# Kernel optimization log

Hardware: AMD Instinct MI355X
Metric: run time of the kernel (lower is better)

Reference implementation:

```python
import jax, jax.numpy as jnp
import numpy as np

INPUT_DIM = 1024
CODEBOOK_DIM = 128
CODEBOOK_SIZE = 8192
B, N = 8, 4096


def setup_inputs() -> dict:
    key = jax.random.key(0)
    k1, k2, k3 = jax.random.split(key, 3)
    x = jax.random.normal(k1, (B, N, INPUT_DIM), dtype=jnp.float32)
    # xavier_normal_: std = sqrt(2 / (fan_in + fan_out))
    xavier_std = float(np.sqrt(2.0 / (INPUT_DIM + CODEBOOK_DIM)))
    random_projection = jax.random.normal(k2, (INPUT_DIM, CODEBOOK_DIM), dtype=jnp.float32) * xavier_std
    codebook = jax.random.normal(k3, (CODEBOOK_SIZE, CODEBOOK_DIM), dtype=jnp.float32)
    return {"x": x, "random_projection": random_projection, "codebook": codebook}


def reference(x, random_projection, codebook):
    # random projection: [B, N, D] @ [D, E] -> [B, N, E]
    proj = jnp.einsum("bnd,de->bne", x, random_projection)
    b, n, e = proj.shape
    flat = proj.reshape(b * n, e)  # [BN, E]
    eps = 1e-12  # matches torch F.normalize default eps
    nx = flat / jnp.maximum(jnp.linalg.norm(flat, axis=1, keepdims=True), eps)
    ncb = codebook / jnp.maximum(jnp.linalg.norm(codebook, axis=1, keepdims=True), eps)
    # squared euclidean distances [K, BN]; argmin of d^2 == argmin of cdist
    d2 = (
        jnp.sum(ncb * ncb, axis=1)[:, None]
        + jnp.sum(nx * nx, axis=1)[None, :]
        - 2.0 * (ncb @ nx.T)
    )
    nearest = jnp.argmin(d2, axis=0)  # [BN]
    return nearest.reshape(b, n).astype(jnp.int32)
```

## Files before the change

### kernel.cpp

```cpp
#include <hip/hip_runtime.h>
#include <math.h>
#include <float.h>
#include <limits.h>

#define BN      32768
#define D_IN    1024
#define E_DIM   128
#define CB_N    8192

typedef _Float16 f16x8 __attribute__((ext_vector_type(8)));
typedef _Float16 f16x4 __attribute__((ext_vector_type(4)));
typedef float    f32x4 __attribute__((ext_vector_type(4)));


__global__ __launch_bounds__(256) void pack_cb_kernel(
    const float* __restrict__ cb, _Float16* __restrict__ ph,
    _Float16* __restrict__ pl) {
    __shared__ float L[16][129];
    const int t = threadIdx.x;
    const int g = blockIdx.x;

    const int c = t >> 4, p = t & 15;
    const float4 v0 = *(const float4*)&cb[(size_t)(g * 16 + c) * E_DIM + p * 8];
    const float4 v1 = *(const float4*)&cb[(size_t)(g * 16 + c) * E_DIM + p * 8 + 4];
    float ss = v0.x * v0.x + v0.y * v0.y + v0.z * v0.z + v0.w * v0.w
             + v1.x * v1.x + v1.y * v1.y + v1.z * v1.z + v1.w * v1.w;
#pragma unroll
    for (int m = 1; m < 16; m <<= 1) ss += __shfl_xor(ss, m);
    const float inv = 256.0f / fmaxf(sqrtf(ss), 1e-12f);

    L[c][p * 8 + 0] = v0.x * inv; L[c][p * 8 + 1] = v0.y * inv;
    L[c][p * 8 + 2] = v0.z * inv; L[c][p * 8 + 3] = v0.w * inv;
    L[c][p * 8 + 4] = v1.x * inv; L[c][p * 8 + 5] = v1.y * inv;
    L[c][p * 8 + 6] = v1.z * inv; L[c][p * 8 + 7] = v1.w * inv;
    __syncthreads();

    const int kb = t >> 6, lane = t & 63;
    const int quad = (lane >> 4), col = lane & 15;
    f16x8 h, l;
#pragma unroll
    for (int j = 0; j < 8; ++j) {
        const float v = L[col][kb * 32 + quad * 8 + j];
        const _Float16 hv = (_Float16)v;
        h[j] = hv;
        l[j] = (_Float16)(v - (float)hv);
    }
    const size_t off = ((size_t)(g * 4 + kb) * 64 + lane) * 8;
    *(f16x8*)&ph[off] = h;
    *(f16x8*)&pl[off] = l;
}

__global__ __launch_bounds__(64) void pack_rp_kernel(
    const float* __restrict__ rp, _Float16* __restrict__ rph,
    _Float16* __restrict__ rpl) {
    const int b = blockIdx.x;
    const int kb = b >> 3, nt = b & 7;
    const int lane = threadIdx.x;
    const int quad = lane >> 4, col = lane & 15;
    f16x8 h, l;
#pragma unroll
    for (int j = 0; j < 8; ++j) {
        const float v = rp[(size_t)(kb * 32 + quad * 8 + j) * E_DIM + nt * 16 + col] * 64.0f;
        const _Float16 hv = (_Float16)v;
        h[j] = hv;
        l[j] = (_Float16)(v - (float)hv);
    }
    const size_t off = ((size_t)b * 64 + lane) * 8;
    *(f16x8*)&rph[off] = h;
    *(f16x8*)&rpl[off] = l;
}

#define PAD_ROW 40
#define PPITCH  132

__global__ __launch_bounds__(256, 2) void fused_kernel(
    const float* __restrict__ x,
    const _Float16* __restrict__ rph, const _Float16* __restrict__ rpl,
    const _Float16* __restrict__ ph, const _Float16* __restrict__ pl,
    int* __restrict__ out) {
    __shared__ _Float16 Ah[64 * PAD_ROW];
    __shared__ _Float16 Al[64 * PAD_ROW];
    __shared__ float    P[64 * PPITCH];
    __shared__ float    ls[4][32];
    __shared__ int      li[4][32];

    const int tid  = threadIdx.x;
    const int lane = tid & 63;
    const int w    = tid >> 6;
    const int quad = lane >> 4, col = lane & 15;
    const int qb   = blockIdx.x * 64;

    const int srow = tid >> 3;
    const int skc  = (tid & 7) * 4;

    f32x4 acc[4][2];
#pragma unroll
    for (int mt = 0; mt < 4; ++mt)
#pragma unroll
        for (int h = 0; h < 2; ++h) acc[mt][h] = (f32x4){0.f, 0.f, 0.f, 0.f};

    float4 pre[2];
#pragma unroll
    for (int i = 0; i < 2; ++i)
        pre[i] = *(const float4*)&x[(size_t)(qb + srow + 32 * i) * D_IN + skc];

    for (int kb = 0; kb < 32; ++kb) {
#pragma unroll
        for (int i = 0; i < 2; ++i) {
            const float vv[4] = {pre[i].x, pre[i].y, pre[i].z, pre[i].w};
            f16x4 h4, l4;
#pragma unroll
            for (int j = 0; j < 4; ++j) {
                const float v = vv[j] * 512.0f;
                const _Float16 hv = (_Float16)v;
                h4[j] = hv;
                l4[j] = (_Float16)(v - (float)hv);
            }
            const int base = (srow + 32 * i) * PAD_ROW + skc;
            *(f16x4*)&Ah[base] = h4;
            *(f16x4*)&Al[base] = l4;
        }
        __syncthreads();

        if (kb + 1 < 32) {
#pragma unroll
            for (int i = 0; i < 2; ++i)
                pre[i] = *(const float4*)&x[(size_t)(qb + srow + 32 * i) * D_IN + (kb + 1) * 32 + skc];
        }

        f16x8 bh1[2], bl1[2];
#pragma unroll
        for (int h = 0; h < 2; ++h) {
            const int nt = w * 2 + h;
            const size_t off = ((size_t)(kb * 8 + nt) * 64 + lane) * 8;
            bh1[h] = *(const f16x8*)&rph[off];
            bl1[h] = *(const f16x8*)&rpl[off];
        }

        f16x8 ah1[4], al1[4];
#pragma unroll
        for (int mt = 0; mt < 4; ++mt) {
            const int base = (mt * 16 + col) * PAD_ROW + quad * 8;
            ah1[mt] = *(const f16x8*)&Ah[base];
            al1[mt] = *(const f16x8*)&Al[base];
        }

#pragma unroll
        for (int mt = 0; mt < 4; ++mt)
#pragma unroll
            for (int h = 0; h < 2; ++h)
                acc[mt][h] = __builtin_amdgcn_mfma_f32_16x16x32_f16(ah1[mt], bh1[h], acc[mt][h], 0, 0, 0);
#pragma unroll
        for (int mt = 0; mt < 4; ++mt)
#pragma unroll
            for (int h = 0; h < 2; ++h)
                acc[mt][h] = __builtin_amdgcn_mfma_f32_16x16x32_f16(ah1[mt], bl1[h], acc[mt][h], 0, 0, 0);
#pragma unroll
        for (int mt = 0; mt < 4; ++mt)
#pragma unroll
            for (int h = 0; h < 2; ++h)
                acc[mt][h] = __builtin_amdgcn_mfma_f32_16x16x32_f16(al1[mt], bh1[h], acc[mt][h], 0, 0, 0);

        __syncthreads();
    }

#pragma unroll
    for (int mt = 0; mt < 4; ++mt)
#pragma unroll
        for (int h = 0; h < 2; ++h)
#pragma unroll
            for (int r = 0; r < 4; ++r) {
                const int row = mt * 16 + quad * 4 + r;
                const int cc  = w * 32 + h * 16 + col;
                P[row * PPITCH + cc] = acc[mt][h][r] * (1.0f / 2048.0f);
            }
    __syncthreads();

    const int wq = w >> 1;
    const int wc = w & 1;

    f16x8 ah[2][4], al[2][4];
#pragma unroll
    for (int mt2 = 0; mt2 < 2; ++mt2)
#pragma unroll
        for (int kb = 0; kb < 4; ++kb) {
            const int base = (wq * 32 + mt2 * 16 + col) * PPITCH + kb * 32 + quad * 8;
            const float4 v0 = *(const float4*)&P[base];
            const float4 v1 = *(const float4*)&P[base + 4];
            const float vv[8] = {v0.x, v0.y, v0.z, v0.w, v1.x, v1.y, v1.z, v1.w};
            f16x8 hh, ll;
#pragma unroll
            for (int j = 0; j < 8; ++j) {
                const _Float16 hv = (_Float16)vv[j];
                hh[j] = hv;
                ll[j] = (_Float16)(vv[j] - (float)hv);
            }
            ah[mt2][kb] = hh;
            al[mt2][kb] = ll;
        }

    float bs[8];
    int   bi[8];
#pragma unroll
    for (int s = 0; s < 8; ++s) { bs[s] = -FLT_MAX; bi[s] = 0; }

    const int g0 = wc * 256;

    f16x8 bh[2][4], bl[2][4];
#pragma unroll
    for (int kb = 0; kb < 4; ++kb) {
        const size_t off = ((size_t)(g0 * 4 + kb) * 64 + lane) * 8;
        bh[0][kb] = *(const f16x8*)&ph[off];
        bl[0][kb] = *(const f16x8*)&pl[off];
    }

#pragma unroll 2
    for (int t = 0; t < 256; ++t) {
        const int cur = t & 1, nxt = cur ^ 1;
        if (t + 1 < 256) {
            const int gn = g0 + t + 1;
#pragma unroll
            for (int kb = 0; kb < 4; ++kb) {
                const size_t off = ((size_t)(gn * 4 + kb) * 64 + lane) * 8;
                bh[nxt][kb] = *(const f16x8*)&ph[off];
                bl[nxt][kb] = *(const f16x8*)&pl[off];
            }
        }

        f32x4 sacc[2];
#pragma unroll
        for (int mt2 = 0; mt2 < 2; ++mt2) sacc[mt2] = (f32x4){0.f, 0.f, 0.f, 0.f};

#pragma unroll
        for (int kb = 0; kb < 4; ++kb)
#pragma unroll
            for (int mt2 = 0; mt2 < 2; ++mt2)
                sacc[mt2] = __builtin_amdgcn_mfma_f32_16x16x32_f16(ah[mt2][kb], bh[cur][kb], sacc[mt2], 0, 0, 0);
#pragma unroll
        for (int kb = 0; kb < 4; ++kb)
#pragma unroll
            for (int mt2 = 0; mt2 < 2; ++mt2)
                sacc[mt2] = __builtin_amdgcn_mfma_f32_16x16x32_f16(ah[mt2][kb], bl[cur][kb], sacc[mt2], 0, 0, 0);
#pragma unroll
        for (int kb = 0; kb < 4; ++kb)
#pragma unroll
            for (int mt2 = 0; mt2 < 2; ++mt2)
                sacc[mt2] = __builtin_amdgcn_mfma_f32_16x16x32_f16(al[mt2][kb], bh[cur][kb], sacc[mt2], 0, 0, 0);

        const int code = (g0 + t) * 16 + col;
#pragma unroll
        for (int mt2 = 0; mt2 < 2; ++mt2)
#pragma unroll
            for (int r = 0; r < 4; ++r) {
                const float v = sacc[mt2][r];
                const int s = mt2 * 4 + r;
                if (v > bs[s]) { bs[s] = v; bi[s] = code; }
            }
    }

#pragma unroll
    for (int s = 0; s < 8; ++s) {
#pragma unroll
        for (int m = 1; m < 16; m <<= 1) {
            const float os = __shfl_xor(bs[s], m);
            const int   oi = __shfl_xor(bi[s], m);
            if (os > bs[s] || (os == bs[s] && oi < bi[s])) { bs[s] = os; bi[s] = oi; }
        }
    }

    if (col == 0) {
#pragma unroll
        for (int mt2 = 0; mt2 < 2; ++mt2)
#pragma unroll
            for (int r = 0; r < 4; ++r) {
                ls[w][mt2 * 16 + quad * 4 + r] = bs[mt2 * 4 + r];
                li[w][mt2 * 16 + quad * 4 + r] = bi[mt2 * 4 + r];
            }
    }
    __syncthreads();

    if (tid < 64) {
        const int q   = tid;
        const int wq2 = q >> 5;
        const int q32 = q & 31;
        float s = ls[wq2 * 2 + 0][q32];
        int   i = li[wq2 * 2 + 0][q32];
        const float os = ls[wq2 * 2 + 1][q32];
        if (os > s) { s = os; i = li[wq2 * 2 + 1][q32]; }
        out[qb + q] = i;
    }
}

extern "C" void kernel_launch(void* const* d_in, const int* in_sizes, int n_in,
                              void* d_out, int out_size, void* d_ws, size_t ws_size,
                              hipStream_t stream) {
    const float* x  = (const float*)d_in[0];
    const float* rp = (const float*)d_in[1];
    const float* cb = (const float*)d_in[2];
    int* out = (int*)d_out;

    _Float16* ph  = (_Float16*)d_ws;
    _Float16* pl  = ph  + (size_t)CB_N * E_DIM;
    _Float16* rph = pl  + (size_t)CB_N * E_DIM;
    _Float16* rpl = rph + (size_t)D_IN * E_DIM;

    pack_cb_kernel<<<CB_N / 16, 256, 0, stream>>>(cb, ph, pl);
    pack_rp_kernel<<<256, 64, 0, stream>>>(rp, rph, rpl);
    fused_kernel<<<BN / 64, 256, 0, stream>>>(x, rph, rpl, ph, pl, out);
}
```

Before: 395.6 us.

## Double query tile per block and share codebook tiles via LDS across waves

The fused kernel now handles 128 queries per block instead of 64, with each wave owning 32 queries and scanning the full codebook. Codebook hi/lo tiles are loaded cooperatively into a double-buffered LDS buffer rather than each wave fetching its own half from global memory. This removes the cross-wave argmin merge and the two pack kernels are merged into one launch. In exchange it uses more registers (launch bounds 1), adds a block-wide sync per codebook tile, and halves the grid to 256 blocks.

```diff
diff --git a/kernel.cpp b/kernel.cpp
--- a/kernel.cpp
+++ b/kernel.cpp
@@ -13,101 +13,99 @@
 typedef float    f32x4 __attribute__((ext_vector_type(4)));
 
 
-__global__ __launch_bounds__(256) void pack_cb_kernel(
-    const float* __restrict__ cb, _Float16* __restrict__ ph,
-    _Float16* __restrict__ pl) {
-    __shared__ float L[16][129];
+__global__ __launch_bounds__(256) void pack_kernel(
+    const float* __restrict__ cb, const float* __restrict__ rp,
+    _Float16* __restrict__ ph, _Float16* __restrict__ pl,
+    _Float16* __restrict__ rph, _Float16* __restrict__ rpl) {
     const int t = threadIdx.x;
-    const int g = blockIdx.x;
-
-    const int c = t >> 4, p = t & 15;
-    const float4 v0 = *(const float4*)&cb[(size_t)(g * 16 + c) * E_DIM + p * 8];
-    const float4 v1 = *(const float4*)&cb[(size_t)(g * 16 + c) * E_DIM + p * 8 + 4];
-    float ss = v0.x * v0.x + v0.y * v0.y + v0.z * v0.z + v0.w * v0.w
-             + v1.x * v1.x + v1.y * v1.y + v1.z * v1.z + v1.w * v1.w;
-#pragma unroll
-    for (int m = 1; m < 16; m <<= 1) ss += __shfl_xor(ss, m);
-    const float inv = 256.0f / fmaxf(sqrtf(ss), 1e-12f);
-
-    L[c][p * 8 + 0] = v0.x * inv; L[c][p * 8 + 1] = v0.y * inv;
-    L[c][p * 8 + 2] = v0.z * inv; L[c][p * 8 + 3] = v0.w * inv;
-    L[c][p * 8 + 4] = v1.x * inv; L[c][p * 8 + 5] = v1.y * inv;
-    L[c][p * 8 + 6] = v1.z * inv; L[c][p * 8 + 7] = v1.w * inv;
-    __syncthreads();
-
-    const int kb = t >> 6, lane = t & 63;
-    const int quad = (lane >> 4), col = lane & 15;
-    f16x8 h, l;
-#pragma unroll
-    for (int j = 0; j < 8; ++j) {
-        const float v = L[col][kb * 32 + quad * 8 + j];
-        const _Float16 hv = (_Float16)v;
-        h[j] = hv;
-        l[j] = (_Float16)(v - (float)hv);
-    }
-    const size_t off = ((size_t)(g * 4 + kb) * 64 + lane) * 8;
-    *(f16x8*)&ph[off] = h;
-    *(f16x8*)&pl[off] = l;
+    if (blockIdx.x < 512) {
+        __shared__ float L[16][129];
+        const int g = blockIdx.x;
+        const int c = t >> 4, p = t & 15;
+        const float4 v0 = *(const float4*)&cb[(size_t)(g * 16 + c) * E_DIM + p * 8];
+        const float4 v1 = *(const float4*)&cb[(size_t)(g * 16 + c) * E_DIM + p * 8 + 4];
+        float ss = v0.x * v0.x + v0.y * v0.y + v0.z * v0.z + v0.w * v0.w
+                 + v1.x * v1.x + v1.y * v1.y + v1.z * v1.z + v1.w * v1.w;
+#pragma unroll
+        for (int m = 1; m < 16; m <<= 1) ss += __shfl_xor(ss, m);
+        const float inv = 256.0f / fmaxf(sqrtf(ss), 1e-12f);
+
+        L[c][p * 8 + 0] = v0.x * inv; L[c][p * 8 + 1] = v0.y * inv;
+        L[c][p * 8 + 2] = v0.z * inv; L[c][p * 8 + 3] = v0.w * inv;
+        L[c][p * 8 + 4] = v1.x * inv; L[c][p * 8 + 5] = v1.y * inv;
+        L[c][p * 8 + 6] = v1.z * inv; L[c][p * 8 + 7] = v1.w * inv;
+        __syncthreads();
+
+        const int kb = t >> 6, lane = t & 63;
+        const int quad = (lane >> 4), col = lane & 15;
+        f16x8 h, l;
+#pragma unroll
+        for (int j = 0; j < 8; ++j) {
+            const float v = L[col][kb * 32 + quad * 8 + j];
+            const _Float16 hv = (_Float16)v;
+            h[j] = hv;
+            l[j] = (_Float16)(v - (float)hv);
+        }
+        const size_t off = ((size_t)(g * 4 + kb) * 64 + lane) * 8;
+        *(f16x8*)&ph[off] = h;
+        *(f16x8*)&pl[off] = l;
+    } else {
+        const int w = t >> 6, lane = t & 63;
+        const int b = (blockIdx.x - 512) * 4 + w;
+        const int kb = b >> 3, nt = b & 7;
+        const int quad = lane >> 4, col = lane & 15;
+        f16x8 h, l;
+#pragma unroll
+        for (int j = 0; j < 8; ++j) {
+            const float v = rp[(size_t)(kb * 32 + quad * 8 + j) * E_DIM + nt * 16 + col] * 64.0f;
+            const _Float16 hv = (_Float16)v;
+            h[j] = hv;
+            l[j] = (_Float16)(v - (float)hv);
+        }
+        const size_t off = ((size_t)b * 64 + lane) * 8;
+        *(f16x8*)&rph[off] = h;
+        *(f16x8*)&rpl[off] = l;
+    }
 }
 
-__global__ __launch_bounds__(64) void pack_rp_kernel(
-    const float* __restrict__ rp, _Float16* __restrict__ rph,
-    _Float16* __restrict__ rpl) {
-    const int b = blockIdx.x;
-    const int kb = b >> 3, nt = b & 7;
-    const int lane = threadIdx.x;
-    const int quad = lane >> 4, col = lane & 15;
-    f16x8 h, l;
-#pragma unroll
-    for (int j = 0; j < 8; ++j) {
-        const float v = rp[(size_t)(kb * 32 + quad * 8 + j) * E_DIM + nt * 16 + col] * 64.0f;
-        const _Float16 hv = (_Float16)v;
-        h[j] = hv;
-        l[j] = (_Float16)(v - (float)hv);
-    }
-    const size_t off = ((size_t)b * 64 + lane) * 8;
-    *(f16x8*)&rph[off] = h;
-    *(f16x8*)&rpl[off] = l;
-}
-
 #define PAD_ROW 40
-#define PPITCH  132
-
-__global__ __launch_bounds__(256, 2) void fused_kernel(
+#define HPITCH  132
+
+__global__ __launch_bounds__(256, 1) void fused_kernel(
     const float* __restrict__ x,
     const _Float16* __restrict__ rph, const _Float16* __restrict__ rpl,
     const _Float16* __restrict__ ph, const _Float16* __restrict__ pl,
     int* __restrict__ out) {
-    __shared__ _Float16 Ah[64 * PAD_ROW];
-    __shared__ _Float16 Al[64 * PAD_ROW];
-    __shared__ float    P[64 * PPITCH];
-    __shared__ float    ls[4][32];
-    __shared__ int      li[4][32];
+    __shared__ __align__(16) unsigned char smem[32768];
+    _Float16* Ah = (_Float16*)smem;
+    _Float16* Al = (_Float16*)(smem + 10240);
+    float*    Pq = (float*)smem;
+    _Float16* Bb = (_Float16*)smem;
 
     const int tid  = threadIdx.x;
     const int lane = tid & 63;
     const int w    = tid >> 6;
     const int quad = lane >> 4, col = lane & 15;
-    const int qb   = blockIdx.x * 64;
-
-    const int srow = tid >> 3;
-    const int skc  = (tid & 7) * 4;
-
-    f32x4 acc[4][2];
-#pragma unroll
-    for (int mt = 0; mt < 4; ++mt)
+    const int qb   = blockIdx.x * 128;
+
+    const int srow = tid >> 1;
+    const int scol = (tid & 1) * 16;
+
+    f32x4 acc[8][2];
+#pragma unroll
+    for (int mt = 0; mt < 8; ++mt)
 #pragma unroll
         for (int h = 0; h < 2; ++h) acc[mt][h] = (f32x4){0.f, 0.f, 0.f, 0.f};
 
-    float4 pre[2];
-#pragma unroll
-    for (int i = 0; i < 2; ++i)
-        pre[i] = *(const float4*)&x[(size_t)(qb + srow + 32 * i) * D_IN + skc];
+    float4 pre[4];
+#pragma unroll
+    for (int c = 0; c < 4; ++c)
+        pre[c] = *(const float4*)&x[(size_t)(qb + srow) * D_IN + scol + c * 4];
 
     for (int kb = 0; kb < 32; ++kb) {
 #pragma unroll
-        for (int i = 0; i < 2; ++i) {
-            const float vv[4] = {pre[i].x, pre[i].y, pre[i].z, pre[i].w};
+        for (int c = 0; c < 4; ++c) {
+            const float vv[4] = {pre[c].x, pre[c].y, pre[c].z, pre[c].w};
             f16x4 h4, l4;
 #pragma unroll
             for (int j = 0; j < 4; ++j) {
@@ -116,7 +114,7 @@
                 h4[j] = hv;
                 l4[j] = (_Float16)(v - (float)hv);
             }
-            const int base = (srow + 32 * i) * PAD_ROW + skc;
+            const int base = srow * PAD_ROW + scol + c * 4;
             *(f16x4*)&Ah[base] = h4;
             *(f16x4*)&Al[base] = l4;
         }
@@ -124,8 +122,8 @@
 
         if (kb + 1 < 32) {
 #pragma unroll
-            for (int i = 0; i < 2; ++i)
-                pre[i] = *(const float4*)&x[(size_t)(qb + srow + 32 * i) * D_IN + (kb + 1) * 32 + skc];
+            for (int c = 0; c < 4; ++c)
+                pre[c] = *(const float4*)&x[(size_t)(qb + srow) * D_IN + (kb + 1) * 32 + scol + c * 4];
         }
 
         f16x8 bh1[2], bl1[2];
@@ -137,26 +135,26 @@
             bl1[h] = *(const f16x8*)&rpl[off];
         }
 
-        f16x8 ah1[4], al1[4];
-#pragma unroll
-        for (int mt = 0; mt < 4; ++mt) {
+        f16x8 ah1[8], al1[8];
+#pragma unroll
+        for (int mt = 0; mt < 8; ++mt) {
             const int base = (mt * 16 + col) * PAD_ROW + quad * 8;
             ah1[mt] = *(const f16x8*)&Ah[base];
             al1[mt] = *(const f16x8*)&Al[base];
         }
 
 #pragma unroll
-        for (int mt = 0; mt < 4; ++mt)
+        for (int mt = 0; mt < 8; ++mt)
 #pragma unroll
             for (int h = 0; h < 2; ++h)
                 acc[mt][h] = __builtin_amdgcn_mfma_f32_16x16x32_f16(ah1[mt], bh1[h], acc[mt][h], 0, 0, 0);
 #pragma unroll
-        for (int mt = 0; mt < 4; ++mt)
+        for (int mt = 0; mt < 8; ++mt)
 #pragma unroll
             for (int h = 0; h < 2; ++h)
                 acc[mt][h] = __builtin_amdgcn_mfma_f32_16x16x32_f16(ah1[mt], bl1[h], acc[mt][h], 0, 0, 0);
 #pragma unroll
-        for (int mt = 0; mt < 4; ++mt)
+        for (int mt = 0; mt < 8; ++mt)
 #pragma unroll
             for (int h = 0; h < 2; ++h)
                 acc[mt][h] = __builtin_amdgcn_mfma_f32_16x16x32_f16(al1[mt], bh1[h], acc[mt][h], 0, 0, 0);
@@ -164,98 +162,121 @@
         __syncthreads();
     }
 
-#pragma unroll
-    for (int mt = 0; mt < 4; ++mt)
-#pragma unroll
-        for (int h = 0; h < 2; ++h)
-#pragma unroll
-            for (int r = 0; r < 4; ++r) {
-                const int row = mt * 16 + quad * 4 + r;
-                const int cc  = w * 32 + h * 16 + col;
-                P[row * PPITCH + cc] = acc[mt][h][r] * (1.0f / 2048.0f);
-            }
-    __syncthreads();
-
-    const int wq = w >> 1;
-    const int wc = w & 1;
-
-    f16x8 ah[2][4], al[2][4];
-#pragma unroll
-    for (int mt2 = 0; mt2 < 2; ++mt2)
-#pragma unroll
-        for (int kb = 0; kb < 4; ++kb) {
-            const int base = (wq * 32 + mt2 * 16 + col) * PPITCH + kb * 32 + quad * 8;
-            const float4 v0 = *(const float4*)&P[base];
-            const float4 v1 = *(const float4*)&P[base + 4];
-            const float vv[8] = {v0.x, v0.y, v0.z, v0.w, v1.x, v1.y, v1.z, v1.w};
-            f16x8 hh, ll;
-#pragma unroll
-            for (int j = 0; j < 8; ++j) {
-                const _Float16 hv = (_Float16)vv[j];
-                hh[j] = hv;
-                ll[j] = (_Float16)(vv[j] - (float)hv);
-            }
-            ah[mt2][kb] = hh;
-            al[mt2][kb] = ll;
-        }
+    f16x8 stg[4];
+#pragma unroll
+    for (int r = 0; r < 4; ++r) {
+        const int cc = w * 4 + r;
+        const _Float16* src = (cc < 8) ? &ph[(size_t)0 * 4096 + cc * 512 + lane * 8]
+                                       : &pl[(size_t)0 * 4096 + (cc - 8) * 512 + lane * 8];
+        stg[r] = *(const f16x8*)src;
+    }
+
+    f16x8 ahF[2][4], alF[2][4];
+#pragma unroll
+    for (int i = 0; i < 4; ++i) {
+#pragma unroll
+        for (int m2 = 0; m2 < 2; ++m2) {
+            const int mt = i * 2 + m2;
+#pragma unroll
+            for (int h = 0; h < 2; ++h)
+#pragma unroll
+                for (int r = 0; r < 4; ++r)
+                    Pq[(m2 * 16 + quad * 4 + r) * HPITCH + w * 32 + h * 16 + col]
+                        = acc[mt][h][r] * (1.0f / 2048.0f);
+        }
+        __syncthreads();
+        if (w == i) {
+#pragma unroll
+            for (int mt2 = 0; mt2 < 2; ++mt2)
+#pragma unroll
+                for (int kbb = 0; kbb < 4; ++kbb) {
+                    const int base = (mt2 * 16 + col) * HPITCH + kbb * 32 + quad * 8;
+                    const float4 v0 = *(const float4*)&Pq[base];
+                    const float4 v1 = *(const float4*)&Pq[base + 4];
+                    const float vv[8] = {v0.x, v0.y, v0.z, v0.w, v1.x, v1.y, v1.z, v1.w};
+                    f16x8 hh, ll;
+#pragma unroll
+                    for (int j = 0; j < 8; ++j) {
+                        const _Float16 hv = (_Float16)vv[j];
+                        hh[j] = hv;
+                        ll[j] = (_Float16)(vv[j] - (float)hv);
+                    }
+                    ahF[mt2][kbb] = hh;
+                    alF[mt2][kbb] = ll;
+                }
+        }
+        __syncthreads();
+    }
 
     float bs[8];
     int   bi[8];
 #pragma unroll
     for (int s = 0; s < 8; ++s) { bs[s] = -FLT_MAX; bi[s] = 0; }
 
-    const int g0 = wc * 256;
-
-    f16x8 bh[2][4], bl[2][4];
-#pragma unroll
-    for (int kb = 0; kb < 4; ++kb) {
-        const size_t off = ((size_t)(g0 * 4 + kb) * 64 + lane) * 8;
-        bh[0][kb] = *(const f16x8*)&ph[off];
-        bl[0][kb] = *(const f16x8*)&pl[off];
-    }
-
-#pragma unroll 2
+#pragma unroll
+    for (int r = 0; r < 4; ++r) {
+        const int cc = w * 4 + r;
+        *(f16x8*)&Bb[cc * 512 + lane * 8] = stg[r];
+    }
+    __syncthreads();
+
     for (int t = 0; t < 256; ++t) {
-        const int cur = t & 1, nxt = cur ^ 1;
+        f16x8 nxt[4];
         if (t + 1 < 256) {
-            const int gn = g0 + t + 1;
-#pragma unroll
-            for (int kb = 0; kb < 4; ++kb) {
-                const size_t off = ((size_t)(gn * 4 + kb) * 64 + lane) * 8;
-                bh[nxt][kb] = *(const f16x8*)&ph[off];
-                bl[nxt][kb] = *(const f16x8*)&pl[off];
-            }
-        }
-
-        f32x4 sacc[2];
-#pragma unroll
-        for (int mt2 = 0; mt2 < 2; ++mt2) sacc[mt2] = (f32x4){0.f, 0.f, 0.f, 0.f};
-
-#pragma unroll
-        for (int kb = 0; kb < 4; ++kb)
-#pragma unroll
-            for (int mt2 = 0; mt2 < 2; ++mt2)
-                sacc[mt2] = __builtin_amdgcn_mfma_f32_16x16x32_f16(ah[mt2][kb], bh[cur][kb], sacc[mt2], 0, 0, 0);
-#pragma unroll
-        for (int kb = 0; kb < 4; ++kb)
-#pragma unroll
-            for (int mt2 = 0; mt2 < 2; ++mt2)
-                sacc[mt2] = __builtin_amdgcn_mfma_f32_16x16x32_f16(ah[mt2][kb], bl[cur][kb], sacc[mt2], 0, 0, 0);
-#pragma unroll
-        for (int kb = 0; kb < 4; ++kb)
-#pragma unroll
-            for (int mt2 = 0; mt2 < 2; ++mt2)
-                sacc[mt2] = __builtin_amdgcn_mfma_f32_16x16x32_f16(al[mt2][kb], bh[cur][kb], sacc[mt2], 0, 0, 0);
-
-        const int code = (g0 + t) * 16 + col;
-#pragma unroll
-        for (int mt2 = 0; mt2 < 2; ++mt2)
 #pragma unroll
             for (int r = 0; r < 4; ++r) {
-                const float v = sacc[mt2][r];
-                const int s = mt2 * 4 + r;
-                if (v > bs[s]) { bs[s] = v; bi[s] = code; }
-            }
+                const int cc = w * 4 + r;
+                const _Float16* src = (cc < 8)
+                    ? &ph[(size_t)(t + 1) * 4096 + cc * 512 + lane * 8]
+                    : &pl[(size_t)(t + 1) * 4096 + (cc - 8) * 512 + lane * 8];
+                nxt[r] = *(const f16x8*)src;
+            }
+        }
+
+        const int bufo = (t & 1) * 8192;
+#pragma unroll
+        for (int ct = 0; ct < 2; ++ct) {
+            f16x8 bh[4], bl[4];
+#pragma unroll
+            for (int kbb = 0; kbb < 4; ++kbb) {
+                bh[kbb] = *(const f16x8*)&Bb[bufo + (ct * 4 + kbb) * 512 + lane * 8];
+                bl[kbb] = *(const f16x8*)&Bb[bufo + 4096 + (ct * 4 + kbb) * 512 + lane * 8];
+            }
+
+            f32x4 s0 = (f32x4){0.f, 0.f, 0.f, 0.f};
+            f32x4 s1 = (f32x4){0.f, 0.f, 0.f, 0.f};
+#pragma unroll
+            for (int kbb = 0; kbb < 4; ++kbb) {
+                s0 = __builtin_amdgcn_mfma_f32_16x16x32_f16(ahF[0][kbb], bh[kbb], s0, 0, 0, 0);
+                s1 = __builtin_amdgcn_mfma_f32_16x16x32_f16(ahF[1][kbb], bh[kbb], s1, 0, 0, 0);
+            }
+#pragma unroll
+            for (int kbb = 0; kbb < 4; ++kbb) {
+                s0 = __builtin_amdgcn_mfma_f32_16x16x32_f16(ahF[0][kbb], bl[kbb], s0, 0, 0, 0);
+                s1 = __builtin_amdgcn_mfma_f32_16x16x32_f16(ahF[1][kbb], bl[kbb], s1, 0, 0, 0);
+            }
+#pragma unroll
+            for (int kbb = 0; kbb < 4; ++kbb) {
+                s0 = __builtin_amdgcn_mfma_f32_16x16x32_f16(alF[0][kbb], bh[kbb], s0, 0, 0, 0);
+                s1 = __builtin_amdgcn_mfma_f32_16x16x32_f16(alF[1][kbb], bh[kbb], s1, 0, 0, 0);
+            }
+
+            const int code = (t * 2 + ct) * 16 + col;
+#pragma unroll
+            for (int r = 0; r < 4; ++r) {
+                if (s0[r] > bs[r])     { bs[r] = s0[r];     bi[r] = code; }
+                if (s1[r] > bs[4 + r]) { bs[4 + r] = s1[r]; bi[4 + r] = code; }
+            }
+        }
+
+        if (t + 1 < 256) {
+#pragma unroll
+            for (int r = 0; r < 4; ++r) {
+                const int cc = w * 4 + r;
+                *(f16x8*)&Bb[((t + 1) & 1) * 8192 + cc * 512 + lane * 8] = nxt[r];
+            }
+        }
+        __syncthreads();
     }
 
 #pragma unroll
@@ -272,22 +293,8 @@
 #pragma unroll
         for (int mt2 = 0; mt2 < 2; ++mt2)
 #pragma unroll
-            for (int r = 0; r < 4; ++r) {
-                ls[w][mt2 * 16 + quad * 4 + r] = bs[mt2 * 4 + r];
-                li[w][mt2 * 16 + quad * 4 + r] = bi[mt2 * 4 + r];
-            }
-    }
-    __syncthreads();
-
-    if (tid < 64) {
-        const int q   = tid;
-        const int wq2 = q >> 5;
-        const int q32 = q & 31;
-        float s = ls[wq2 * 2 + 0][q32];
-        int   i = li[wq2 * 2 + 0][q32];
-        const float os = ls[wq2 * 2 + 1][q32];
-        if (os > s) { s = os; i = li[wq2 * 2 + 1][q32]; }
-        out[qb + q] = i;
+            for (int r = 0; r < 4; ++r)
+                out[qb + w * 32 + mt2 * 16 + quad * 4 + r] = bi[mt2 * 4 + r];
     }
 }
 
@@ -304,7 +311,6 @@
     _Float16* rph = pl  + (size_t)CB_N * E_DIM;
     _Float16* rpl = rph + (size_t)D_IN * E_DIM;
 
-    pack_cb_kernel<<<CB_N / 16, 256, 0, stream>>>(cb, ph, pl);
-    pack_rp_kernel<<<256, 64, 0, stream>>>(rp, rph, rpl);
-    fused_kernel<<<BN / 64, 256, 0, stream>>>(x, rph, rpl, ph, pl, out);
+    pack_kernel<<<576, 256, 0, stream>>>(cb, rp, ph, pl, rph, rpl);
+    fused_kernel<<<BN / 128, 256, 0, stream>>>(x, rph, rpl, ph, pl, out);
 }
```

Result: slower. 438.8 us (+10.9%).

## Split codebook across all four waves and merge pack kernels into one

Applied to the files above, without the earlier changes.

Each wave now scores all 64 query rows against a quarter of the codebook, instead of 32 rows against half. Each codebook fragment loaded from global memory then feeds 4 M-tiles rather than 2, so total codebook traffic per block is halved. The cost is more registers (16 A fragments per wave plus 16 best-score slots) and a 4-way final merge. The two pack kernels are also fused into one launch, and the first codebook prefetch is moved before the barrier.

```diff
diff --git a/kernel.cpp b/kernel.cpp
--- a/kernel.cpp
+++ b/kernel.cpp
@@ -13,61 +13,59 @@
 typedef float    f32x4 __attribute__((ext_vector_type(4)));
 
 
-__global__ __launch_bounds__(256) void pack_cb_kernel(
-    const float* __restrict__ cb, _Float16* __restrict__ ph,
-    _Float16* __restrict__ pl) {
-    __shared__ float L[16][129];
+__global__ __launch_bounds__(256) void pack_kernel(
+    const float* __restrict__ cb, const float* __restrict__ rp,
+    _Float16* __restrict__ ph, _Float16* __restrict__ pl,
+    _Float16* __restrict__ rph, _Float16* __restrict__ rpl) {
     const int t = threadIdx.x;
-    const int g = blockIdx.x;
-
-    const int c = t >> 4, p = t & 15;
-    const float4 v0 = *(const float4*)&cb[(size_t)(g * 16 + c) * E_DIM + p * 8];
-    const float4 v1 = *(const float4*)&cb[(size_t)(g * 16 + c) * E_DIM + p * 8 + 4];
-    float ss = v0.x * v0.x + v0.y * v0.y + v0.z * v0.z + v0.w * v0.w
-             + v1.x * v1.x + v1.y * v1.y + v1.z * v1.z + v1.w * v1.w;
-#pragma unroll
-    for (int m = 1; m < 16; m <<= 1) ss += __shfl_xor(ss, m);
-    const float inv = 256.0f / fmaxf(sqrtf(ss), 1e-12f);
-
-    L[c][p * 8 + 0] = v0.x * inv; L[c][p * 8 + 1] = v0.y * inv;
-    L[c][p * 8 + 2] = v0.z * inv; L[c][p * 8 + 3] = v0.w * inv;
-    L[c][p * 8 + 4] = v1.x * inv; L[c][p * 8 + 5] = v1.y * inv;
-    L[c][p * 8 + 6] = v1.z * inv; L[c][p * 8 + 7] = v1.w * inv;
-    __syncthreads();
-
-    const int kb = t >> 6, lane = t & 63;
-    const int quad = (lane >> 4), col = lane & 15;
-    f16x8 h, l;
-#pragma unroll
-    for (int j = 0; j < 8; ++j) {
-        const float v = L[col][kb * 32 + quad * 8 + j];
-        const _Float16 hv = (_Float16)v;
-        h[j] = hv;
-        l[j] = (_Float16)(v - (float)hv);
-    }
-    const size_t off = ((size_t)(g * 4 + kb) * 64 + lane) * 8;
-    *(f16x8*)&ph[off] = h;
-    *(f16x8*)&pl[off] = l;
-}
-
-__global__ __launch_bounds__(64) void pack_rp_kernel(
-    const float* __restrict__ rp, _Float16* __restrict__ rph,
-    _Float16* __restrict__ rpl) {
-    const int b = blockIdx.x;
-    const int kb = b >> 3, nt = b & 7;
-    const int lane = threadIdx.x;
-    const int quad = lane >> 4, col = lane & 15;
-    f16x8 h, l;
-#pragma unroll
-    for (int j = 0; j < 8; ++j) {
-        const float v = rp[(size_t)(kb * 32 + quad * 8 + j) * E_DIM + nt * 16 + col] * 64.0f;
-        const _Float16 hv = (_Float16)v;
-        h[j] = hv;
-        l[j] = (_Float16)(v - (float)hv);
-    }
-    const size_t off = ((size_t)b * 64 + lane) * 8;
-    *(f16x8*)&rph[off] = h;
-    *(f16x8*)&rpl[off] = l;
+    if (blockIdx.x < 512) {
+        __shared__ float L[16][129];
+        const int g = blockIdx.x;
+        const int c = t >> 4, p = t & 15;
+        const float4 v0 = *(const float4*)&cb[(size_t)(g * 16 + c) * E_DIM + p * 8];
+        const float4 v1 = *(const float4*)&cb[(size_t)(g * 16 + c) * E_DIM + p * 8 + 4];
+        float ss = v0.x * v0.x + v0.y * v0.y + v0.z * v0.z + v0.w * v0.w
+                 + v1.x * v1.x + v1.y * v1.y + v1.z * v1.z + v1.w * v1.w;
+#pragma unroll
+        for (int m = 1; m < 16; m <<= 1) ss += __shfl_xor(ss, m);
+        const float inv = 256.0f / fmaxf(sqrtf(ss), 1e-12f);
+
+        L[c][p * 8 + 0] = v0.x * inv; L[c][p * 8 + 1] = v0.y * inv;
+        L[c][p * 8 + 2] = v0.z * inv; L[c][p * 8 + 3] = v0.w * inv;
+        L[c][p * 8 + 4] = v1.x * inv; L[c][p * 8 + 5] = v1.y * inv;
+        L[c][p * 8 + 6] = v1.z * inv; L[c][p * 8 + 7] = v1.w * inv;
+        __syncthreads();
+
+        const int kb = t >> 6, lane = t & 63;
+        const int quad = (lane >> 4), col = lane & 15;
+        f16x8 h, l;
+#pragma unroll
+        for (int j = 0; j < 8; ++j) {
+            const float v = L[col][kb * 32 + quad * 8 + j];
+            const _Float16 hv = (_Float16)v;
+            h[j] = hv;
+            l[j] = (_Float16)(v - (float)hv);
+        }
+        const size_t off = ((size_t)(g * 4 + kb) * 64 + lane) * 8;
+        *(f16x8*)&ph[off] = h;
+        *(f16x8*)&pl[off] = l;
+    } else {
+        const int w = t >> 6, lane = t & 63;
+        const int b = (blockIdx.x - 512) * 4 + w;
+        const int kb = b >> 3, nt = b & 7;
+        const int quad = lane >> 4, col = lane & 15;
+        f16x8 h, l;
+#pragma unroll
+        for (int j = 0; j < 8; ++j) {
+            const float v = rp[(size_t)(kb * 32 + quad * 8 + j) * E_DIM + nt * 16 + col] * 64.0f;
+            const _Float16 hv = (_Float16)v;
+            h[j] = hv;
+            l[j] = (_Float16)(v - (float)hv);
+        }
+        const size_t off = ((size_t)b * 64 + lane) * 8;
+        *(f16x8*)&rph[off] = h;
+        *(f16x8*)&rpl[off] = l;
+    }
 }
 
 #define PAD_ROW 40
@@ -81,8 +79,8 @@
     __shared__ _Float16 Ah[64 * PAD_ROW];
     __shared__ _Float16 Al[64 * PAD_ROW];
     __shared__ float    P[64 * PPITCH];
-    __shared__ float    ls[4][32];
-    __shared__ int      li[4][32];
+    __shared__ float    ls[4][64];
+    __shared__ int      li[4][64];
 
     const int tid  = threadIdx.x;
     const int lane = tid & 63;
@@ -169,22 +167,26 @@
 #pragma unroll
         for (int h = 0; h < 2; ++h)
 #pragma unroll
-            for (int r = 0; r < 4; ++r) {
-                const int row = mt * 16 + quad * 4 + r;
-                const int cc  = w * 32 + h * 16 + col;
-                P[row * PPITCH + cc] = acc[mt][h][r] * (1.0f / 2048.0f);
-            }
+            for (int r = 0; r < 4; ++r)
+                P[(mt * 16 + quad * 4 + r) * PPITCH + w * 32 + h * 16 + col]
+                    = acc[mt][h][r] * (1.0f / 2048.0f);
+
+    const int g0 = w * 128;
+    f16x8 bh[2][4], bl[2][4];
+#pragma unroll
+    for (int kb = 0; kb < 4; ++kb) {
+        const size_t off = ((size_t)(g0 * 4 + kb) * 64 + lane) * 8;
+        bh[0][kb] = *(const f16x8*)&ph[off];
+        bl[0][kb] = *(const f16x8*)&pl[off];
+    }
     __syncthreads();
 
-    const int wq = w >> 1;
-    const int wc = w & 1;
-
-    f16x8 ah[2][4], al[2][4];
-#pragma unroll
-    for (int mt2 = 0; mt2 < 2; ++mt2)
-#pragma unroll
-        for (int kb = 0; kb < 4; ++kb) {
-            const int base = (wq * 32 + mt2 * 16 + col) * PPITCH + kb * 32 + quad * 8;
+    f16x8 ahF[4][4], alF[4][4];
+#pragma unroll
+    for (int mt = 0; mt < 4; ++mt)
+#pragma unroll
+        for (int kbb = 0; kbb < 4; ++kbb) {
+            const int base = (mt * 16 + col) * PPITCH + kbb * 32 + quad * 8;
             const float4 v0 = *(const float4*)&P[base];
             const float4 v1 = *(const float4*)&P[base + 4];
             const float vv[8] = {v0.x, v0.y, v0.z, v0.w, v1.x, v1.y, v1.z, v1.w};
@@ -195,29 +197,19 @@
                 hh[j] = hv;
                 ll[j] = (_Float16)(vv[j] - (float)hv);
             }
-            ah[mt2][kb] = hh;
-            al[mt2][kb] = ll;
-        }
-
-    float bs[8];
-    int   bi[8];
-#pragma unroll
-    for (int s = 0; s < 8; ++s) { bs[s] = -FLT_MAX; bi[s] = 0; }
-
-    const int g0 = wc * 256;
-
-    f16x8 bh[2][4], bl[2][4];
-#pragma unroll
-    for (int kb = 0; kb < 4; ++kb) {
-        const size_t off = ((size_t)(g0 * 4 + kb) * 64 + lane) * 8;
-        bh[0][kb] = *(const f16x8*)&ph[off];
-        bl[0][kb] = *(const f16x8*)&pl[off];
-    }
+            ahF[mt][kbb] = hh;
+            alF[mt][kbb] = ll;
+        }
+
+    float bs[16];
+    int   bi[16];
+#pragma unroll
+    for (int s = 0; s < 16; ++s) { bs[s] = -FLT_MAX; bi[s] = 0; }
 
 #pragma unroll 2
-    for (int t = 0; t < 256; ++t) {
+    for (int t = 0; t < 128; ++t) {
         const int cur = t & 1, nxt = cur ^ 1;
-        if (t + 1 < 256) {
+        if (t + 1 < 128) {
             const int gn = g0 + t + 1;
 #pragma unroll
             for (int kb = 0; kb < 4; ++kb) {
@@ -227,39 +219,39 @@
             }
         }
 
-        f32x4 sacc[2];
-#pragma unroll
-        for (int mt2 = 0; mt2 < 2; ++mt2) sacc[mt2] = (f32x4){0.f, 0.f, 0.f, 0.f};
+        f32x4 sacc[4];
+#pragma unroll
+        for (int mt = 0; mt < 4; ++mt) sacc[mt] = (f32x4){0.f, 0.f, 0.f, 0.f};
 
 #pragma unroll
         for (int kb = 0; kb < 4; ++kb)
 #pragma unroll
-            for (int mt2 = 0; mt2 < 2; ++mt2)
-                sacc[mt2] = __builtin_amdgcn_mfma_f32_16x16x32_f16(ah[mt2][kb], bh[cur][kb], sacc[mt2], 0, 0, 0);
+            for (int mt = 0; mt < 4; ++mt)
+                sacc[mt] = __builtin_amdgcn_mfma_f32_16x16x32_f16(ahF[mt][kb], bh[cur][kb], sacc[mt], 0, 0, 0);
 #pragma unroll
         for (int kb = 0; kb < 4; ++kb)
 #pragma unroll
-            for (int mt2 = 0; mt2 < 2; ++mt2)
-                sacc[mt2] = __builtin_amdgcn_mfma_f32_16x16x32_f16(ah[mt2][kb], bl[cur][kb], sacc[mt2], 0, 0, 0);
+            for (int mt = 0; mt < 4; ++mt)
+                sacc[mt] = __builtin_amdgcn_mfma_f32_16x16x32_f16(ahF[mt][kb], bl[cur][kb], sacc[mt], 0, 0, 0);
 #pragma unroll
         for (int kb = 0; kb < 4; ++kb)
 #pragma unroll
-            for (int mt2 = 0; mt2 < 2; ++mt2)
-                sacc[mt2] = __builtin_amdgcn_mfma_f32_16x16x32_f16(al[mt2][kb], bh[cur][kb], sacc[mt2], 0, 0, 0);
+            for (int mt = 0; mt < 4; ++mt)
+                sacc[mt] = __builtin_amdgcn_mfma_f32_16x16x32_f16(alF[mt][kb], bh[cur][kb], sacc[mt], 0, 0, 0);
 
         const int code = (g0 + t) * 16 + col;
 #pragma unroll
-        for (int mt2 = 0; mt2 < 2; ++mt2)
+        for (int mt = 0; mt < 4; ++mt)
 #pragma unroll
             for (int r = 0; r < 4; ++r) {
-                const float v = sacc[mt2][r];
-                const int s = mt2 * 4 + r;
+                const float v = sacc[mt][r];
+                const int s = mt * 4 + r;
                 if (v > bs[s]) { bs[s] = v; bi[s] = code; }
             }
     }
 
 #pragma unroll
-    for (int s = 0; s < 8; ++s) {
+    for (int s = 0; s < 16; ++s) {
 #pragma unroll
         for (int m = 1; m < 16; m <<= 1) {
             const float os = __shfl_xor(bs[s], m);
@@ -270,24 +262,24 @@
 
     if (col == 0) {
 #pragma unroll
-        for (int mt2 = 0; mt2 < 2; ++mt2)
+        for (int mt = 0; mt < 4; ++mt)
 #pragma unroll
             for (int r = 0; r < 4; ++r) {
-                ls[w][mt2 * 16 + quad * 4 + r] = bs[mt2 * 4 + r];
-                li[w][mt2 * 16 + quad * 4 + r] = bi[mt2 * 4 + r];
+                ls[w][mt * 16 + quad * 4 + r] = bs[mt * 4 + r];
+                li[w][mt * 16 + quad * 4 + r] = bi[mt * 4 + r];
             }
     }
     __syncthreads();
 
     if (tid < 64) {
-        const int q   = tid;
-        const int wq2 = q >> 5;
-        const int q32 = q & 31;
-        float s = ls[wq2 * 2 + 0][q32];
-        int   i = li[wq2 * 2 + 0][q32];
-        const float os = ls[wq2 * 2 + 1][q32];
-        if (os > s) { s = os; i = li[wq2 * 2 + 1][q32]; }
-        out[qb + q] = i;
+        float s = ls[0][tid];
+        int   i = li[0][tid];
+#pragma unroll
+        for (int ww = 1; ww < 4; ++ww) {
+            const float os = ls[ww][tid];
+            if (os > s) { s = os; i = li[ww][tid]; }
+        }
+        out[qb + tid] = i;
     }
 }
 
@@ -304,7 +296,6 @@
     _Float16* rph = pl  + (size_t)CB_N * E_DIM;
     _Float16* rpl = rph + (size_t)D_IN * E_DIM;
 
-    pack_cb_kernel<<<CB_N / 16, 256, 0, stream>>>(cb, ph, pl);
-    pack_rp_kernel<<<256, 64, 0, stream>>>(rp, rph, rpl);
+    pack_kernel<<<576, 256, 0, stream>>>(cb, rp, ph, pl, rph, rpl);
     fused_kernel<<<BN / 64, 256, 0, stream>>>(x, rph, rpl, ph, pl, out);
 }
```

Result: no change. 399.9 us (+1.1%).
